# Optimization experiments

Hardware: AMD Instinct MI355X
Metric: run time of the kernel (lower is better)

Reference implementation:

```python
import jax, jax.numpy as jnp
import numpy as np

B, S, D, H, E = 4, 2048, 2048, 4096, 8
TOP_K = 2
ENTROPY_WEIGHT = 0.1
MAX_USAGE_RATIO = 0.3


def setup_inputs() -> dict:
    key = jax.random.key(0)
    k0, k1, k2 = jax.random.split(key, 3)
    x = jax.random.normal(k0, (B, S, D), dtype=jnp.float32)
    gate_w = jax.random.normal(k1, (E, D), dtype=jnp.float32) * 0.02
    gate_b = jnp.zeros((E,), dtype=jnp.float32)
    expert_w = jax.random.normal(k2, (E, H, D), dtype=jnp.float32) * 0.02
    expert_b = jnp.zeros((E, H), dtype=jnp.float32)
    return {"x": x, "gate_w": gate_w, "gate_b": gate_b,
            "expert_w": expert_w, "expert_b": expert_b}


def reference(x, gate_w, gate_b, expert_w, expert_b):
    b, s, d = x.shape
    e, h, _ = expert_w.shape
    n = b * s
    xf = x.reshape(n, d)

    # gating
    gate_logits = xf @ gate_w.T + gate_b              # (N, E)
    gate_probs = jax.nn.softmax(gate_logits, axis=-1)
    entropy = (-jnp.sum(gate_probs * jnp.log(gate_probs + 1e-10), axis=-1)).mean()
    entropy_loss = ENTROPY_WEIGHT * entropy

    # top-k dispatch weights
    topk_probs, topk_idx = jax.lax.top_k(gate_probs, TOP_K)   # (N, K)
    combine = jnp.sum(jax.nn.one_hot(topk_idx, e, dtype=xf.dtype)
                      * topk_probs[..., None], axis=1)        # (N, E)

    # per-expert linear + weighted combine (loop over small fixed E)
    out = jnp.zeros((n, h), dtype=xf.dtype)
    for ei in range(e):
        out = out + combine[:, ei:ei + 1] * (xf @ expert_w[ei].T + expert_b[ei])

    # usage penalty (this batch's routing counts)
    counts = jnp.sum(jax.nn.one_hot(topk_idx, e, dtype=jnp.float32), axis=(0, 1))
    usage_ratios = counts / n
    overuse_penalty = jnp.sum(jax.nn.relu(usage_ratios - MAX_USAGE_RATIO))

    return out.reshape(b, s, h), entropy_loss + overuse_penalty
```

## Files before the change

### kernel.cpp

```cpp
#include <hip/hip_runtime.h>

constexpr int N_TOK = 8192;
constexpr int D_IN  = 2048;
constexpr int H_OUT = 4096;
constexpr int NEXP  = 8;
constexpr float ENT_W = 0.1f;
constexpr float MAX_USAGE = 0.3f;

constexpr int TM = 128;
constexpr int TH = 128;
constexpr int BK = 32;
constexpr int NKT = D_IN / BK;
constexpr int TILES_H = H_OUT / TH;
constexpr int REGION  = 8192;
constexpr int BUFSZ   = TM * BK;
constexpr int MAXTILES = N_TOK * 2 / TM + NEXP;
constexpr int GRID_GEMM = MAXTILES * TILES_H;

typedef __attribute__((ext_vector_type(8))) short bf16x8;
typedef __attribute__((ext_vector_type(4))) float f32x4;

__device__ __forceinline__ short f2bf(float f) {
    unsigned u = __float_as_uint(f);
    u += 0x7FFF + ((u >> 16) & 1);
    return (short)(u >> 16);
}

__device__ __forceinline__ void gload16(const void* g, void* l) {
    __builtin_amdgcn_global_load_lds(
        (const __attribute__((address_space(1))) unsigned int*)g,
        (__attribute__((address_space(3))) unsigned int*)l, 16, 0, 0);
}

__global__ __launch_bounds__(256) void gate_cvt_kernel(
    const float* __restrict__ x, const float* __restrict__ gate_w,
    const float* __restrict__ gate_b, float* __restrict__ ent_partial,
    short* __restrict__ xb,
    const float* __restrict__ expert_w, short* __restrict__ wb,
    int* __restrict__ cursors, int* __restrict__ tok_list,
    float* __restrict__ w_list)
{
    __shared__ float ent_s[4];
    __shared__ int   lcnt[NEXP], lbase[NEXP];
    __shared__ int   pick_e[4][2], pick_p[4][2];
    __shared__ float pick_w[4][2];

    const int wv = threadIdx.x >> 6;
    const int lane = threadIdx.x & 63;
    const int t = blockIdx.x * 4 + wv;

    if (threadIdx.x < NEXP) lcnt[threadIdx.x] = 0;

    float acc[NEXP];
#pragma unroll
    for (int e = 0; e < NEXP; ++e) acc[e] = 0.f;

    const float4* xr = (const float4*)(x + (size_t)t * D_IN);
    short* xbr = xb + (size_t)t * D_IN;
#pragma unroll
    for (int i = 0; i < D_IN / 256; ++i) {
        float4 xv = xr[lane + i * 64];
        short4 s4;
        s4.x = f2bf(xv.x); s4.y = f2bf(xv.y); s4.z = f2bf(xv.z); s4.w = f2bf(xv.w);
        *(short4*)(xbr + i * 256 + lane * 4) = s4;
#pragma unroll
        for (int e = 0; e < NEXP; ++e) {
            float4 gv = ((const float4*)(gate_w + e * D_IN))[lane + i * 64];
            acc[e] += xv.x * gv.x + xv.y * gv.y + xv.z * gv.z + xv.w * gv.w;
        }
    }
#pragma unroll
    for (int e = 0; e < NEXP; ++e)
#pragma unroll
        for (int m = 32; m >= 1; m >>= 1) acc[e] += __shfl_xor(acc[e], m, 64);

    __syncthreads();
    if (lane == 0) {
        float lg[NEXP], p[NEXP];
        float mx = -1e30f;
#pragma unroll
        for (int e = 0; e < NEXP; ++e) { lg[e] = acc[e] + gate_b[e]; mx = fmaxf(mx, lg[e]); }
        float s = 0.f;
#pragma unroll
        for (int e = 0; e < NEXP; ++e) { p[e] = expf(lg[e] - mx); s += p[e]; }
        float inv = 1.f / s;
        float ent = 0.f;
#pragma unroll
        for (int e = 0; e < NEXP; ++e) { p[e] *= inv; ent -= p[e] * logf(p[e] + 1e-10f); }
        int e1 = 0; float b1 = p[0];
#pragma unroll
        for (int e = 1; e < NEXP; ++e) if (p[e] > b1) { b1 = p[e]; e1 = e; }
        int e2 = (e1 == 0) ? 1 : 0; float b2 = p[e2];
#pragma unroll
        for (int e = 0; e < NEXP; ++e)
            if (e != e1 && e != ((e1 == 0) ? 1 : 0) && p[e] > b2) { b2 = p[e]; e2 = e; }
        int p0 = atomicAdd(&lcnt[e1], 1);
        int p1 = atomicAdd(&lcnt[e2], 1);
        pick_e[wv][0] = e1; pick_p[wv][0] = p0; pick_w[wv][0] = b1;
        pick_e[wv][1] = e2; pick_p[wv][1] = p1; pick_w[wv][1] = b2;
        ent_s[wv] = ent;
    }
    __syncthreads();
    if (threadIdx.x < NEXP)
        lbase[threadIdx.x] = lcnt[threadIdx.x] ?
            atomicAdd(&cursors[threadIdx.x], lcnt[threadIdx.x]) : 0;
    if (threadIdx.x == 0)
        ent_partial[blockIdx.x] = ent_s[0] + ent_s[1] + ent_s[2] + ent_s[3];
    __syncthreads();
    if (lane == 0) {
#pragma unroll
        for (int k = 0; k < 2; ++k) {
            int e = pick_e[wv][k];
            int dst = e * REGION + lbase[e] + pick_p[wv][k];
            tok_list[dst] = t;
            w_list[dst] = pick_w[wv][k];
        }
    }

    const int total = NEXP << 20;
    int stride = gridDim.x * 256;
    for (int d = blockIdx.x * 256 + threadIdx.x; d < total; d += stride) {
        int e    = d >> 20;
        int th   = (d >> 15) & 31;
        int kt   = (d >> 9) & 63;
        int row  = (d >> 2) & 127;
        int q    = d & 3;
        int h = th * 128 + row;
        int k = kt * 32 + q * 8;
        const float4* s = (const float4*)(expert_w + ((size_t)e * H_OUT + h) * D_IN + k);
        float4 a = s[0], b = s[1];
        bf16x8 v;
        v[0] = f2bf(a.x); v[1] = f2bf(a.y); v[2] = f2bf(a.z); v[3] = f2bf(a.w);
        v[4] = f2bf(b.x); v[5] = f2bf(b.y); v[6] = f2bf(b.z); v[7] = f2bf(b.w);
        *(bf16x8*)(wb + (size_t)d * 8) = v;
    }
}

__global__ __launch_bounds__(64) void plan_kernel(
    const int* __restrict__ counts, int* __restrict__ ntiles,
    int* __restrict__ desc_e, int* __restrict__ desc_base,
    int* __restrict__ desc_valid)
{
    if (threadIdx.x == 0) {
        int n = 0;
        for (int e = 0; e < NEXP; ++e) {
            int cnt = counts[e];
            for (int i = 0; i * TM < cnt; ++i) {
                desc_e[n] = e;
                desc_base[n] = e * REGION + i * TM;
                int v = cnt - i * TM;
                desc_valid[n] = v < TM ? v : TM;
                ++n;
            }
        }
        ntiles[0] = n;
    }
}

__global__ __launch_bounds__(256) void finalize_kernel(
    const int* __restrict__ counts, const float* __restrict__ ent_partial,
    float* __restrict__ loss_out)
{
    __shared__ float red[256];
    float s = 0.f;
    for (int i = threadIdx.x; i < N_TOK / 4; i += 256) s += ent_partial[i];
    red[threadIdx.x] = s;
    __syncthreads();
    for (int st = 128; st > 0; st >>= 1) {
        if (threadIdx.x < st) red[threadIdx.x] += red[threadIdx.x + st];
        __syncthreads();
    }
    if (threadIdx.x == 0) {
        float loss = ENT_W * red[0] / (float)N_TOK;
        for (int e = 0; e < NEXP; ++e) {
            float r = (float)counts[e] / (float)N_TOK - MAX_USAGE;
            if (r > 0.f) loss += r;
        }
        loss_out[0] = loss;
    }
}

__global__ __launch_bounds__(256, 4) void moe_gemm(
    const short* __restrict__ xb, const short* __restrict__ wb,
    const float* __restrict__ expert_b, const int* __restrict__ tok_list,
    const float* __restrict__ w_list, const int* __restrict__ ntiles,
    const int* __restrict__ desc_e, const int* __restrict__ desc_base,
    const int* __restrict__ desc_valid, float* __restrict__ out)
{
    const int bid = blockIdx.x;
    const int swz = (bid & 7) * (GRID_GEMM / 8) + (bid >> 3);
    const int tIdx = swz >> 5;
    const int th   = swz & 31;
    if (tIdx >= ntiles[0]) return;

    const int e     = desc_e[tIdx];
    const int base  = desc_base[tIdx];
    const int valid = desc_valid[tIdx];
    const int hbase = th * TH;

    __shared__ __align__(16) short A_s[2][BUFSZ];
    __shared__ __align__(16) short B_s[2][BUFSZ];
    __shared__ int   tok_s[TM];
    __shared__ float wgt_s[TM];

    const int tid = threadIdx.x;
    if (tid < TM) {
        bool v = tid < valid;
        tok_s[tid] = v ? tok_list[base + tid] : tok_list[base];
        wgt_s[tid] = v ? w_list[base + tid] : 0.f;
    }
    __syncthreads();

    const int lane = tid & 63;
    const int wv = tid >> 6;

    const char* asrc[2];
    const char* bsrc[2];
    int dst_off[2];
    const char* bpanel = (const char*)wb +
        ((size_t)(e * TILES_H + th)) * (64 * 8192);
#pragma unroll
    for (int j = 0; j < 2; ++j) {
        int c = wv * 2 + j;
        int r = c * 16 + (lane >> 2);
        int s2 = (lane & 3) ^ ((lane >> 3) & 3);
        asrc[j] = (const char*)(xb + (size_t)tok_s[r] * D_IN) + s2 * 16;
        bsrc[j] = bpanel + c * 1024 + (lane >> 2) * 64 + s2 * 16;
        dst_off[j] = c * 512;
    }

    const int rr = lane & 15, kg = lane >> 4;
    const int wr = wv >> 1, wc = wv & 1;

    int aoff[4], boff[4];
#pragma unroll
    for (int mi = 0; mi < 4; ++mi) {
        int row = wr * 64 + mi * 16 + rr;
        aoff[mi] = row * 32 + (kg ^ ((row >> 1) & 3)) * 8;
        int rowb = wc * 64 + mi * 16 + rr;
        boff[mi] = rowb * 32 + (kg ^ ((rowb >> 1) & 3)) * 8;
    }

    f32x4 acc[4][4] = {};

#define STAGE_KT(buf)                                                      \
    {                                                                      \
        short* Aso = (short*)A_s[buf];                                     \
        short* Bso = (short*)B_s[buf];                                     \
        gload16(asrc[0], Aso + dst_off[0]); asrc[0] += BK * 2;             \
        gload16(bsrc[0], Bso + dst_off[0]); bsrc[0] += 8192;               \
        gload16(asrc[1], Aso + dst_off[1]); asrc[1] += BK * 2;             \
        gload16(bsrc[1], Bso + dst_off[1]); bsrc[1] += 8192;               \
    }

    STAGE_KT(0);
    STAGE_KT(1);
    asm volatile("s_waitcnt vmcnt(4)" ::: "memory");
    __builtin_amdgcn_sched_barrier(0);
    __builtin_amdgcn_s_barrier();

    for (int kt = 0; kt < NKT; ++kt) {
        const short* Ac = A_s[kt & 1];
        const short* Bc = B_s[kt & 1];

        bf16x8 af[4], bv[4];
#pragma unroll
        for (int mi = 0; mi < 4; ++mi) af[mi] = *(const bf16x8*)&Ac[aoff[mi]];
#pragma unroll
        for (int ni = 0; ni < 4; ++ni) bv[ni] = *(const bf16x8*)&Bc[boff[ni]];
        asm volatile("s_waitcnt lgkmcnt(0)" ::: "memory");
        __builtin_amdgcn_sched_barrier(0);
        __builtin_amdgcn_s_barrier();

        if (kt + 2 < NKT) STAGE_KT(kt & 1);

        __builtin_amdgcn_s_setprio(1);
#pragma unroll
        for (int mi = 0; mi < 4; ++mi)
#pragma unroll
            for (int ni = 0; ni < 4; ++ni)
                acc[mi][ni] = __builtin_amdgcn_mfma_f32_16x16x32_bf16(
                    af[mi], bv[ni], acc[mi][ni], 0, 0, 0);
        __builtin_amdgcn_s_setprio(0);

        if (kt + 2 < NKT) {
            asm volatile("s_waitcnt vmcnt(4)" ::: "memory");
        } else if (kt + 1 < NKT) {
            asm volatile("s_waitcnt vmcnt(0)" ::: "memory");
        }
        __builtin_amdgcn_sched_barrier(0);
        __builtin_amdgcn_s_barrier();
    }
#undef STAGE_KT

    const float* bias = expert_b + (size_t)e * H_OUT + hbase;
#pragma unroll
    for (int mi = 0; mi < 4; ++mi) {
#pragma unroll
        for (int ni = 0; ni < 4; ++ni) {
            int col = wc * 64 + ni * 16 + rr;
            float be = bias[col];
#pragma unroll
            for (int i = 0; i < 4; ++i) {
                int r = wr * 64 + mi * 16 + kg * 4 + i;
                if (r < valid) {
                    float val = wgt_s[r] * (acc[mi][ni][i] + be);
                    atomicAdd(&out[(size_t)tok_s[r] * H_OUT + hbase + col], val);
                }
            }
        }
    }
}

extern "C" void kernel_launch(void* const* d_in, const int* in_sizes, int n_in,
                              void* d_out, int out_size, void* d_ws, size_t ws_size,
                              hipStream_t stream) {
    const float* x        = (const float*)d_in[0];
    const float* gate_w   = (const float*)d_in[1];
    const float* gate_b   = (const float*)d_in[2];
    const float* expert_w = (const float*)d_in[3];
    const float* expert_b = (const float*)d_in[4];
    float* out = (float*)d_out;
    char* ws = (char*)d_ws;

    int*   cursors     = (int*)(ws + (128 << 10));
    int*   ntiles      = (int*)(ws + (128 << 10) + 64);
    int*   desc_e      = (int*)(ws + (128 << 10) + 128);
    int*   desc_base   = (int*)(ws + (128 << 10) + 1024);
    int*   desc_valid  = (int*)(ws + (128 << 10) + 2048);
    float* ent_partial = (float*)(ws + (132 << 10));
    int*   tok_list    = (int*)(ws + (160 << 10));
    float* w_list      = (float*)(ws + (416 << 10));
    short* xb          = (short*)(ws + (1ull << 20));
    short* wb          = (short*)(ws + (34ull << 20));

    hipMemsetAsync(cursors, 0, 64, stream);
    hipMemsetAsync(d_out, 0, (size_t)out_size * sizeof(float), stream);

    gate_cvt_kernel<<<N_TOK / 4, 256, 0, stream>>>(
        x, gate_w, gate_b, ent_partial, xb, expert_w, wb,
        cursors, tok_list, w_list);
    plan_kernel<<<1, 64, 0, stream>>>(cursors, ntiles, desc_e, desc_base,
                                      desc_valid);
    moe_gemm<<<GRID_GEMM, 256, 0, stream>>>(
        xb, wb, expert_b, tok_list, w_list, ntiles, desc_e, desc_base,
        desc_valid, out);
    finalize_kernel<<<1, 256, 0, stream>>>(cursors, ent_partial,
                                           out + (size_t)N_TOK * H_OUT);
}
```

Baseline: 660.4 us.

## Use 512-thread GEMM blocks and compute tile plan inline, dropping plan kernel

```diff
diff --git a/kernel.cpp b/kernel.cpp
--- a/kernel.cpp
+++ b/kernel.cpp
@@ -136,27 +136,6 @@
     }
 }
 
-__global__ __launch_bounds__(64) void plan_kernel(
-    const int* __restrict__ counts, int* __restrict__ ntiles,
-    int* __restrict__ desc_e, int* __restrict__ desc_base,
-    int* __restrict__ desc_valid)
-{
-    if (threadIdx.x == 0) {
-        int n = 0;
-        for (int e = 0; e < NEXP; ++e) {
-            int cnt = counts[e];
-            for (int i = 0; i * TM < cnt; ++i) {
-                desc_e[n] = e;
-                desc_base[n] = e * REGION + i * TM;
-                int v = cnt - i * TM;
-                desc_valid[n] = v < TM ? v : TM;
-                ++n;
-            }
-        }
-        ntiles[0] = n;
-    }
-}
-
 __global__ __launch_bounds__(256) void finalize_kernel(
     const int* __restrict__ counts, const float* __restrict__ ent_partial,
     float* __restrict__ loss_out)
@@ -180,22 +159,35 @@
     }
 }
 
-__global__ __launch_bounds__(256, 4) void moe_gemm(
+__global__ __launch_bounds__(512, 6) void moe_gemm(
     const short* __restrict__ xb, const short* __restrict__ wb,
     const float* __restrict__ expert_b, const int* __restrict__ tok_list,
-    const float* __restrict__ w_list, const int* __restrict__ ntiles,
-    const int* __restrict__ desc_e, const int* __restrict__ desc_base,
-    const int* __restrict__ desc_valid, float* __restrict__ out)
+    const float* __restrict__ w_list, const int* __restrict__ cursors,
+    float* __restrict__ out)
 {
     const int bid = blockIdx.x;
     const int swz = (bid & 7) * (GRID_GEMM / 8) + (bid >> 3);
     const int tIdx = swz >> 5;
     const int th   = swz & 31;
-    if (tIdx >= ntiles[0]) return;
-
-    const int e     = desc_e[tIdx];
-    const int base  = desc_base[tIdx];
-    const int valid = desc_valid[tIdx];
+
+    int e = -1, base = 0, valid = 0;
+    {
+        int n = 0;
+        for (int ee = 0; ee < NEXP; ++ee) {
+            int cnt = cursors[ee];
+            int nt = (cnt + TM - 1) / TM;
+            if (tIdx < n + nt) {
+                e = ee;
+                int i = tIdx - n;
+                base = ee * REGION + i * TM;
+                valid = cnt - i * TM;
+                if (valid > TM) valid = TM;
+                break;
+            }
+            n += nt;
+        }
+    }
+    if (e < 0) return;
     const int hbase = th * TH;
 
     __shared__ __align__(16) short A_s[2][BUFSZ];
@@ -214,48 +206,45 @@
     const int lane = tid & 63;
     const int wv = tid >> 6;
 
-    const char* asrc[2];
-    const char* bsrc[2];
-    int dst_off[2];
-    const char* bpanel = (const char*)wb +
-        ((size_t)(e * TILES_H + th)) * (64 * 8192);
-#pragma unroll
-    for (int j = 0; j < 2; ++j) {
-        int c = wv * 2 + j;
-        int r = c * 16 + (lane >> 2);
+    const char* asrc;
+    const char* bsrc;
+    const int dst_off = wv * 512;
+    {
+        int r = wv * 16 + (lane >> 2);
         int s2 = (lane & 3) ^ ((lane >> 3) & 3);
-        asrc[j] = (const char*)(xb + (size_t)tok_s[r] * D_IN) + s2 * 16;
-        bsrc[j] = bpanel + c * 1024 + (lane >> 2) * 64 + s2 * 16;
-        dst_off[j] = c * 512;
+        asrc = (const char*)(xb + (size_t)tok_s[r] * D_IN) + s2 * 16;
+        const char* bpanel = (const char*)wb +
+            ((size_t)(e * TILES_H + th)) * (64 * 8192);
+        bsrc = bpanel + wv * 1024 + (lane >> 2) * 64 + s2 * 16;
     }
 
     const int rr = lane & 15, kg = lane >> 4;
-    const int wr = wv >> 1, wc = wv & 1;
-
-    int aoff[4], boff[4];
+    const int wr = wv >> 2;
+    const int wc = wv & 3;
+
+    int aoff[4], boff[2];
 #pragma unroll
     for (int mi = 0; mi < 4; ++mi) {
         int row = wr * 64 + mi * 16 + rr;
         aoff[mi] = row * 32 + (kg ^ ((row >> 1) & 3)) * 8;
-        int rowb = wc * 64 + mi * 16 + rr;
-        boff[mi] = rowb * 32 + (kg ^ ((rowb >> 1) & 3)) * 8;
-    }
-
-    f32x4 acc[4][4] = {};
+    }
+#pragma unroll
+    for (int ni = 0; ni < 2; ++ni) {
+        int rowb = wc * 32 + ni * 16 + rr;
+        boff[ni] = rowb * 32 + (kg ^ ((rowb >> 1) & 3)) * 8;
+    }
+
+    f32x4 acc[4][2] = {};
 
 #define STAGE_KT(buf)                                                      \
     {                                                                      \
-        short* Aso = (short*)A_s[buf];                                     \
-        short* Bso = (short*)B_s[buf];                                     \
-        gload16(asrc[0], Aso + dst_off[0]); asrc[0] += BK * 2;             \
-        gload16(bsrc[0], Bso + dst_off[0]); bsrc[0] += 8192;               \
-        gload16(asrc[1], Aso + dst_off[1]); asrc[1] += BK * 2;             \
-        gload16(bsrc[1], Bso + dst_off[1]); bsrc[1] += 8192;               \
+        gload16(asrc, (short*)A_s[buf] + dst_off); asrc += BK * 2;         \
+        gload16(bsrc, (short*)B_s[buf] + dst_off); bsrc += 8192;           \
     }
 
     STAGE_KT(0);
     STAGE_KT(1);
-    asm volatile("s_waitcnt vmcnt(4)" ::: "memory");
+    asm volatile("s_waitcnt vmcnt(2)" ::: "memory");
     __builtin_amdgcn_sched_barrier(0);
     __builtin_amdgcn_s_barrier();
 
@@ -263,11 +252,11 @@
         const short* Ac = A_s[kt & 1];
         const short* Bc = B_s[kt & 1];
 
-        bf16x8 af[4], bv[4];
+        bf16x8 af[4], bv[2];
 #pragma unroll
         for (int mi = 0; mi < 4; ++mi) af[mi] = *(const bf16x8*)&Ac[aoff[mi]];
 #pragma unroll
-        for (int ni = 0; ni < 4; ++ni) bv[ni] = *(const bf16x8*)&Bc[boff[ni]];
+        for (int ni = 0; ni < 2; ++ni) bv[ni] = *(const bf16x8*)&Bc[boff[ni]];
         asm volatile("s_waitcnt lgkmcnt(0)" ::: "memory");
         __builtin_amdgcn_sched_barrier(0);
         __builtin_amdgcn_s_barrier();
@@ -278,13 +267,13 @@
 #pragma unroll
         for (int mi = 0; mi < 4; ++mi)
 #pragma unroll
-            for (int ni = 0; ni < 4; ++ni)
+            for (int ni = 0; ni < 2; ++ni)
                 acc[mi][ni] = __builtin_amdgcn_mfma_f32_16x16x32_bf16(
                     af[mi], bv[ni], acc[mi][ni], 0, 0, 0);
         __builtin_amdgcn_s_setprio(0);
 
         if (kt + 2 < NKT) {
-            asm volatile("s_waitcnt vmcnt(4)" ::: "memory");
+            asm volatile("s_waitcnt vmcnt(2)" ::: "memory");
         } else if (kt + 1 < NKT) {
             asm volatile("s_waitcnt vmcnt(0)" ::: "memory");
         }
@@ -294,18 +283,21 @@
 #undef STAGE_KT
 
     const float* bias = expert_b + (size_t)e * H_OUT + hbase;
+    float be[2];
+#pragma unroll
+    for (int ni = 0; ni < 2; ++ni) be[ni] = bias[wc * 32 + ni * 16 + rr];
 #pragma unroll
     for (int mi = 0; mi < 4; ++mi) {
 #pragma unroll
-        for (int ni = 0; ni < 4; ++ni) {
-            int col = wc * 64 + ni * 16 + rr;
-            float be = bias[col];
-#pragma unroll
-            for (int i = 0; i < 4; ++i) {
-                int r = wr * 64 + mi * 16 + kg * 4 + i;
-                if (r < valid) {
-                    float val = wgt_s[r] * (acc[mi][ni][i] + be);
-                    atomicAdd(&out[(size_t)tok_s[r] * H_OUT + hbase + col], val);
+        for (int i = 0; i < 4; ++i) {
+            int r = wr * 64 + mi * 16 + kg * 4 + i;
+            if (r < valid) {
+                float w = wgt_s[r];
+                float* orow = out + (size_t)tok_s[r] * H_OUT + hbase;
+#pragma unroll
+                for (int ni = 0; ni < 2; ++ni) {
+                    int col = wc * 32 + ni * 16 + rr;
+                    atomicAdd(orow + col, w * (acc[mi][ni][i] + be[ni]));
                 }
             }
         }
@@ -324,10 +316,6 @@
     char* ws = (char*)d_ws;
 
     int*   cursors     = (int*)(ws + (128 << 10));
-    int*   ntiles      = (int*)(ws + (128 << 10) + 64);
-    int*   desc_e      = (int*)(ws + (128 << 10) + 128);
-    int*   desc_base   = (int*)(ws + (128 << 10) + 1024);
-    int*   desc_valid  = (int*)(ws + (128 << 10) + 2048);
     float* ent_partial = (float*)(ws + (132 << 10));
     int*   tok_list    = (int*)(ws + (160 << 10));
     float* w_list      = (float*)(ws + (416 << 10));
@@ -340,11 +328,8 @@
     gate_cvt_kernel<<<N_TOK / 4, 256, 0, stream>>>(
         x, gate_w, gate_b, ent_partial, xb, expert_w, wb,
         cursors, tok_list, w_list);
-    plan_kernel<<<1, 64, 0, stream>>>(cursors, ntiles, desc_e, desc_base,
-                                      desc_valid);
-    moe_gemm<<<GRID_GEMM, 256, 0, stream>>>(
-        xb, wb, expert_b, tok_list, w_list, ntiles, desc_e, desc_base,
-        desc_valid, out);
+    moe_gemm<<<GRID_GEMM, 512, 0, stream>>>(
+        xb, wb, expert_b, tok_list, w_list, cursors, out);
     finalize_kernel<<<1, 256, 0, stream>>>(cursors, ent_partial,
                                            out + (size_t)N_TOK * H_OUT);
 }
```

Result: faster. 613.3 us, median of 3 (-7.1%).
